# Kernel optimization log

Hardware: AMD Instinct MI355X
Metric: run time of the kernel (lower is better)

Reference implementation:

```python
import math
import jax
import jax.numpy as jnp
import numpy as np

DIM = 1024
NUM_EXPERTS = 4
CAPACITY = (0.25, 0.25, 0.25, 0.25)
BATCH = 8
NUM_TOKENS = 4096


def setup_inputs() -> dict:
    key = jax.random.key(0)
    k1, k2 = jax.random.split(key)
    input_tokens = jax.random.normal(k1, (BATCH, NUM_TOKENS, DIM), dtype=jnp.float32)
    # torch Linear weight [out_features, in_features], init uniform(-0.02, 0.02), bias zeros
    W = jax.random.uniform(k2, (NUM_EXPERTS, DIM), dtype=jnp.float32, minval=-0.02, maxval=0.02)
    b = jnp.zeros((NUM_EXPERTS,), dtype=jnp.float32)
    return {"input_tokens": input_tokens, "W": W, "b": b}


def reference(input_tokens, W, b):
    # router probs in float32 (autocast disabled in original)
    logits = jnp.einsum('bnd,ed->bne', input_tokens, W) + b  # [B, N, E]
    probs = jax.nn.softmax(logits, axis=-1)

    B, N, _ = probs.shape
    token_mask = jnp.full((B, N), -1, dtype=jnp.int32)
    neg_inf = jnp.float32(-jnp.inf)

    # Sequential expert-preferred assignment, highest expert index first.
    for j in reversed(range(NUM_EXPERTS)):
        capacity = int(math.floor(CAPACITY[j] * N))
        if capacity == 0:
            continue
        r_j = jnp.where(token_mask != -1, neg_inf, probs[:, :, j])  # mask already-assigned tokens
        _, topk_idx = jax.lax.top_k(r_j, capacity)  # [B, capacity]
        # Faithful to torch `token_mask[:, topk_indices] = j`: assigns expert j at the
        # union of selected token positions across ALL batch rows (broadcast over dim 0).
        token_mask = token_mask.at[:, topk_idx.reshape(-1)].set(j)

    token_mask = jnp.where(token_mask == -1, 0, token_mask)
    expert_probs = jnp.take_along_axis(probs, token_mask[..., None], axis=2)[..., 0]  # [B, N]
    return token_mask, expert_probs
```

## Files before the change

### kernel.cpp

```cpp
#include <hip/hip_runtime.h>
#include <math.h>

#define DIM 1024
#define NE 4
#define NTOK 4096
#define NB 8
#define CAP 1024
#define NWAVE 16
#define HSTRIDE 257

typedef float fx4 __attribute__((ext_vector_type(4)));

__global__ __launch_bounds__(256) void probs_kernel(const float* __restrict__ tokens,
                                                    const float* __restrict__ W,
                                                    const float* __restrict__ bias,
                                                    float* __restrict__ probs) {
    __shared__ float4 Wl[NE * 256];
    int tid = threadIdx.x;
    const float4* W4 = (const float4*)W;
    for (int i = tid; i < NE * 256; i += 256) Wl[i] = W4[i];
    __syncthreads();

    int wave = tid >> 6, lane = tid & 63;
    long tok = (long)blockIdx.x * 4 + wave;
    const fx4* t4 = (const fx4*)(tokens + tok * DIM);

    double a0 = 0, a1 = 0, a2 = 0, a3 = 0;
#pragma unroll
    for (int kk = 0; kk < 4; kk++) {
        int c = lane + 64 * kk;
        fx4 v = __builtin_nontemporal_load(&t4[c]);
        float4 w0 = Wl[0 * 256 + c];
        float4 w1 = Wl[1 * 256 + c];
        float4 w2 = Wl[2 * 256 + c];
        float4 w3 = Wl[3 * 256 + c];
        a0 += (double)v.x * w0.x + (double)v.y * w0.y + (double)v.z * w0.z + (double)v.w * w0.w;
        a1 += (double)v.x * w1.x + (double)v.y * w1.y + (double)v.z * w1.z + (double)v.w * w1.w;
        a2 += (double)v.x * w2.x + (double)v.y * w2.y + (double)v.z * w2.z + (double)v.w * w2.w;
        a3 += (double)v.x * w3.x + (double)v.y * w3.y + (double)v.z * w3.z + (double)v.w * w3.w;
    }
#pragma unroll
    for (int off = 32; off > 0; off >>= 1) {
        a0 += __shfl_xor(a0, off);
        a1 += __shfl_xor(a1, off);
        a2 += __shfl_xor(a2, off);
        a3 += __shfl_xor(a3, off);
    }
    if (lane == 0) {
        float f0 = (float)(a0 + (double)bias[0]);
        float f1 = (float)(a1 + (double)bias[1]);
        float f2 = (float)(a2 + (double)bias[2]);
        float f3 = (float)(a3 + (double)bias[3]);
        double m = fmax(fmax((double)f0, (double)f1), fmax((double)f2, (double)f3));
        double e0 = exp((double)f0 - m);
        double e1 = exp((double)f1 - m);
        double e2 = exp((double)f2 - m);
        double e3 = exp((double)f3 - m);
        double s = e0 + e1 + e2 + e3;
        float4 p;
        p.x = (float)(e0 / s);
        p.y = (float)(e1 / s);
        p.z = (float)(e2 / s);
        p.w = (float)(e3 / s);
        ((float4*)probs)[tok] = p;
    }
}


__device__ __forceinline__ unsigned block_exscan_1024(unsigned v, unsigned* wl,
                                                      int tid, unsigned* total) {
    int lane = tid & 63, w = tid >> 6;
    unsigned s = v;
#pragma unroll
    for (int off = 1; off < 64; off <<= 1) {
        unsigned t = __shfl_up(s, off);
        if (lane >= off) s += t;
    }
    if (lane == 63) wl[w] = s;
    __syncthreads();
    if (tid < 64) {
        unsigned x = (tid < 16) ? wl[tid] : 0u;
#pragma unroll
        for (int off = 1; off < 16; off <<= 1) {
            unsigned t = __shfl_up(x, off);
            if (lane >= off) x += t;
        }
        if (tid < 16) wl[tid] = x;
    }
    __syncthreads();
    unsigned waveoff = (w == 0) ? 0u : wl[w - 1];
    unsigned tot = wl[15];
    __syncthreads();
    if (total) *total = tot;
    return waveoff + (s - v);
}

__device__ __forceinline__ void radix_select_regs(const unsigned key[4], unsigned cap,
                                                  unsigned* whist, unsigned* hist,
                                                  unsigned* scanb, unsigned* bcast,
                                                  int tid,
                                                  unsigned* v_out, unsigned* rem_out) {
    int w = tid >> 6;
    unsigned* myh = whist + w * HSTRIDE;
    if (tid == 0) { bcast[0] = 0u; bcast[1] = cap; }
#pragma unroll
    for (int shift = 24; shift >= 0; shift -= 8) {
        for (int i = tid; i < NWAVE * HSTRIDE; i += 1024) whist[i] = 0u;
        __syncthreads();
        unsigned pref = bcast[0], rem = bcast[1];
        bool all = (shift == 24);
#pragma unroll
        for (int k = 0; k < 4; k++) {
            if (all || (key[k] >> (shift + 8)) == pref)
                atomicAdd(&myh[(key[k] >> shift) & 255u], 1u);
        }
        __syncthreads();
        if (tid < 256) {
            unsigned s = 0;
#pragma unroll
            for (int w2 = 0; w2 < NWAVE; w2++) s += whist[w2 * HSTRIDE + tid];
            hist[tid] = s;
        }
        __syncthreads();
        if (tid < 64) {
            unsigned h0 = hist[4 * tid], h1 = hist[4 * tid + 1];
            unsigned h2 = hist[4 * tid + 2], h3 = hist[4 * tid + 3];
            unsigned s3 = h3, s2 = h2 + s3, s1 = h1 + s2, s0 = h0 + s1;
            unsigned t = s0, s = t;
#pragma unroll
            for (int off = 1; off < 64; off <<= 1) {
                unsigned o = __shfl_down(s, off);
                if (tid + off < 64) s += o;
            }
            unsigned E = s - t;
            scanb[4 * tid]     = E + s0;
            scanb[4 * tid + 1] = E + s1;
            scanb[4 * tid + 2] = E + s2;
            scanb[4 * tid + 3] = E + s3;
        }
        __syncthreads();
        if (tid < 256) {
            unsigned incl = scanb[tid];
            unsigned excl = (tid < 255) ? scanb[tid + 1] : 0u;
            if (excl < rem && rem <= incl) {
                bcast[0] = (pref << 8) | (unsigned)tid;
                bcast[1] = rem - excl;
            }
        }
        __syncthreads();
    }
    *v_out = bcast[0];
    *rem_out = bcast[1];
}

__device__ __forceinline__ unsigned mono_key(float p) {
    unsigned bits = __float_as_uint(p);
    return (bits & 0x80000000u) ? ~bits : (bits | 0x80000000u);
}

__device__ __forceinline__ void select_to_bitmap(const unsigned key[4], unsigned* bitmap,
                                                 unsigned* whist, unsigned* hist,
                                                 unsigned* scanb, unsigned* bcast,
                                                 unsigned* wl, int tid) {
    unsigned vstar, rem;
    radix_select_regs(key, CAP, whist, hist, scanb, bcast, tid, &vstar, &rem);
    unsigned loc[4], v = 0;
#pragma unroll
    for (int k = 0; k < 4; k++) { loc[k] = (key[k] == vstar); v += loc[k]; }
    unsigned tot;
    unsigned ex = block_exscan_1024(v, wl, tid, &tot);
#pragma unroll
    for (int k = 0; k < 4; k++) {
        int i = 4 * tid + k;
        bool sel = (key[k] > vstar) || (loc[k] && ex < rem);
        ex += loc[k];
        if (sel) atomicOr(&bitmap[i >> 5], 1u << (i & 31));
    }
    __syncthreads();
}

__global__ __launch_bounds__(1024) void select3_kernel(const float* __restrict__ probs,
                                                       unsigned* __restrict__ selbits) {
    __shared__ unsigned whist[NWAVE * HSTRIDE];
    __shared__ unsigned hist[256], scanb[256], bcast[2];
    __shared__ unsigned bitmap[128];
    __shared__ unsigned wl[17];
    int b = blockIdx.x, tid = threadIdx.x;

    const float4* p4 = (const float4*)probs + (size_t)b * NTOK;
    unsigned key[4];
#pragma unroll
    for (int k = 0; k < 4; k++) key[k] = mono_key(p4[4 * tid + k].w);
    if (tid < 128) bitmap[tid] = 0u;

    select_to_bitmap(key, bitmap, whist, hist, scanb, bcast, wl, tid);

    if (tid < 128) selbits[b * 128 + tid] = bitmap[tid];
}

__global__ __launch_bounds__(1024) void rest_kernel(const float* __restrict__ probs,
                                                    const unsigned* __restrict__ selbits,
                                                    int* __restrict__ finalmask) {
    __shared__ int maskv[NTOK];
    __shared__ unsigned whist[NWAVE * HSTRIDE];
    __shared__ unsigned hist[256], scanb[256], bcast[2];
    __shared__ unsigned bitmap[128];
    __shared__ unsigned wl[17];
    int tid = threadIdx.x;

    if (tid < 128) {
        unsigned u = 0;
#pragma unroll
        for (int bb = 0; bb < NB; bb++) u |= selbits[bb * 128 + tid];
        bitmap[tid] = u;
    }
    __syncthreads();
#pragma unroll
    for (int k = 0; k < 4; k++) {
        int i = tid + k * 1024;
        maskv[i] = ((bitmap[i >> 5] >> (i & 31)) & 1u) ? 3 : -1;
    }
    __syncthreads();

    for (int j = 2; j >= 0; j--) {
        unsigned loc[4], v = 0;
#pragma unroll
        for (int k = 0; k < 4; k++) { loc[k] = (maskv[4 * tid + k] != -1); v += loc[k]; }
        unsigned M;
        unsigned ex = block_exscan_1024(v, wl, tid, &M);
        unsigned U = NTOK - M;

        if (U <= CAP) {
            unsigned need = CAP - U;
#pragma unroll
            for (int k = 0; k < 4; k++) {
                int i = 4 * tid + k;
                bool sel = (!loc[k]) || (ex < need);
                ex += loc[k];
                if (sel) maskv[i] = j;
            }
            __syncthreads();
        } else {
            if (tid < 128) bitmap[tid] = 0u;
            __syncthreads();
            for (int bb = 0; bb < NB; bb++) {
                unsigned k2[4];
#pragma unroll
                for (int k = 0; k < 4; k++) {
                    int i = 4 * tid + k;
                    k2[k] = (maskv[i] != -1)
                                ? 0u
                                : mono_key(probs[((size_t)bb * NTOK + i) * NE + j]);
                }
                select_to_bitmap(k2, bitmap, whist, hist, scanb, bcast, wl, tid);
            }
#pragma unroll
            for (int k = 0; k < 4; k++) {
                int i = 4 * tid + k;
                if ((bitmap[i >> 5] >> (i & 31)) & 1u) maskv[i] = j;
            }
            __syncthreads();
        }
    }

#pragma unroll
    for (int k = 0; k < 4; k++) {
        int i = tid + k * 1024;
        int m = maskv[i];
        finalmask[i] = (m < 0) ? 0 : m;
    }
}

__global__ __launch_bounds__(256) void final_kernel(const float* __restrict__ probs,
                                                    const int* __restrict__ fm,
                                                    float* __restrict__ out) {
    int i = blockIdx.x * 256 + threadIdx.x;
    int n = i & (NTOK - 1);
    int m = fm[n];
    out[i] = (float)m;
    out[NB * NTOK + i] = probs[(size_t)i * NE + m];
}

extern "C" void kernel_launch(void* const* d_in, const int* in_sizes, int n_in,
                              void* d_out, int out_size, void* d_ws, size_t ws_size,
                              hipStream_t stream) {
    const float* tokens = (const float*)d_in[0];
    const float* W      = (const float*)d_in[1];
    const float* bias   = (const float*)d_in[2];
    float* out = (float*)d_out;

    float*    probs   = (float*)d_ws;
    unsigned* selbits = (unsigned*)((char*)d_ws + (size_t)NB * NTOK * NE * sizeof(float));
    int*      fmask   = (int*)(selbits + NB * 128);

    probs_kernel<<<(NB * NTOK) / 4, 256, 0, stream>>>(tokens, W, bias, probs);
    select3_kernel<<<NB, 1024, 0, stream>>>(probs, selbits);
    rest_kernel<<<1, 1024, 0, stream>>>(probs, selbits, fmask);
    final_kernel<<<(NB * NTOK) / 256, 256, 0, stream>>>(probs, fmask, out);
}
```

Measured before the change: 211.4 us.

## Keep router weights in registers and process four tokens per wave with prefetch

The router-probability kernel stops staging W in shared memory and loads each lane's weight slice into registers once. Each wave now handles four tokens and prefetches the next token's row while computing the current one, so the grid shrinks by a factor of four. This aims to drop the per-block shared-memory load and barrier and to hide global load latency for the bandwidth-bound token read. In exchange it uses more registers per thread, which may lower occupancy, and leaves fewer blocks in flight.

Result: no change. 211.6 us (+0.1%).

```diff
diff --git a/kernel.cpp b/kernel.cpp
--- a/kernel.cpp
+++ b/kernel.cpp
@@ -15,54 +15,78 @@
                                                     const float* __restrict__ W,
                                                     const float* __restrict__ bias,
                                                     float* __restrict__ probs) {
-    __shared__ float4 Wl[NE * 256];
-    int tid = threadIdx.x;
-    const float4* W4 = (const float4*)W;
-    for (int i = tid; i < NE * 256; i += 256) Wl[i] = W4[i];
-    __syncthreads();
-
+    int tid  = threadIdx.x;
     int wave = tid >> 6, lane = tid & 63;
-    long tok = (long)blockIdx.x * 4 + wave;
-    const fx4* t4 = (const fx4*)(tokens + tok * DIM);
-
-    double a0 = 0, a1 = 0, a2 = 0, a3 = 0;
-#pragma unroll
-    for (int kk = 0; kk < 4; kk++) {
-        int c = lane + 64 * kk;
-        fx4 v = __builtin_nontemporal_load(&t4[c]);
-        float4 w0 = Wl[0 * 256 + c];
-        float4 w1 = Wl[1 * 256 + c];
-        float4 w2 = Wl[2 * 256 + c];
-        float4 w3 = Wl[3 * 256 + c];
-        a0 += (double)v.x * w0.x + (double)v.y * w0.y + (double)v.z * w0.z + (double)v.w * w0.w;
-        a1 += (double)v.x * w1.x + (double)v.y * w1.y + (double)v.z * w1.z + (double)v.w * w1.w;
-        a2 += (double)v.x * w2.x + (double)v.y * w2.y + (double)v.z * w2.z + (double)v.w * w2.w;
-        a3 += (double)v.x * w3.x + (double)v.y * w3.y + (double)v.z * w3.z + (double)v.w * w3.w;
-    }
-#pragma unroll
-    for (int off = 32; off > 0; off >>= 1) {
-        a0 += __shfl_xor(a0, off);
-        a1 += __shfl_xor(a1, off);
-        a2 += __shfl_xor(a2, off);
-        a3 += __shfl_xor(a3, off);
-    }
-    if (lane == 0) {
-        float f0 = (float)(a0 + (double)bias[0]);
-        float f1 = (float)(a1 + (double)bias[1]);
-        float f2 = (float)(a2 + (double)bias[2]);
-        float f3 = (float)(a3 + (double)bias[3]);
-        double m = fmax(fmax((double)f0, (double)f1), fmax((double)f2, (double)f3));
-        double e0 = exp((double)f0 - m);
-        double e1 = exp((double)f1 - m);
-        double e2 = exp((double)f2 - m);
-        double e3 = exp((double)f3 - m);
-        double s = e0 + e1 + e2 + e3;
-        float4 p;
-        p.x = (float)(e0 / s);
-        p.y = (float)(e1 / s);
-        p.z = (float)(e2 / s);
-        p.w = (float)(e3 / s);
-        ((float4*)probs)[tok] = p;
+
+    const fx4* W4 = (const fx4*)W;
+    fx4 w[NE][4];
+#pragma unroll
+    for (int e = 0; e < NE; e++)
+#pragma unroll
+        for (int k = 0; k < 4; k++)
+            w[e][k] = W4[e * 256 + lane + 64 * k];
+
+    double b0 = (double)bias[0], b1 = (double)bias[1];
+    double b2 = (double)bias[2], b3 = (double)bias[3];
+
+    long tok0 = ((long)blockIdx.x * 4 + wave) * 4;
+
+    fx4 v0, v1, v2, v3;
+    {
+        const fx4* tp = (const fx4*)(tokens + tok0 * DIM);
+        v0 = __builtin_nontemporal_load(&tp[lane]);
+        v1 = __builtin_nontemporal_load(&tp[lane + 64]);
+        v2 = __builtin_nontemporal_load(&tp[lane + 128]);
+        v3 = __builtin_nontemporal_load(&tp[lane + 192]);
+    }
+
+#pragma unroll
+    for (int t = 0; t < 4; t++) {
+        fx4 n0, n1, n2, n3;
+        if (t < 3) {
+            const fx4* np = (const fx4*)(tokens + (tok0 + t + 1) * DIM);
+            n0 = __builtin_nontemporal_load(&np[lane]);
+            n1 = __builtin_nontemporal_load(&np[lane + 64]);
+            n2 = __builtin_nontemporal_load(&np[lane + 128]);
+            n3 = __builtin_nontemporal_load(&np[lane + 192]);
+        }
+
+        double a0 = 0, a1 = 0, a2 = 0, a3 = 0;
+        fx4 vv[4] = {v0, v1, v2, v3};
+#pragma unroll
+        for (int k = 0; k < 4; k++) {
+            fx4 v = vv[k];
+            a0 += (double)v.x * w[0][k].x + (double)v.y * w[0][k].y + (double)v.z * w[0][k].z + (double)v.w * w[0][k].w;
+            a1 += (double)v.x * w[1][k].x + (double)v.y * w[1][k].y + (double)v.z * w[1][k].z + (double)v.w * w[1][k].w;
+            a2 += (double)v.x * w[2][k].x + (double)v.y * w[2][k].y + (double)v.z * w[2][k].z + (double)v.w * w[2][k].w;
+            a3 += (double)v.x * w[3][k].x + (double)v.y * w[3][k].y + (double)v.z * w[3][k].z + (double)v.w * w[3][k].w;
+        }
+#pragma unroll
+        for (int off = 32; off > 0; off >>= 1) {
+            a0 += __shfl_xor(a0, off);
+            a1 += __shfl_xor(a1, off);
+            a2 += __shfl_xor(a2, off);
+            a3 += __shfl_xor(a3, off);
+        }
+        if (lane == 0) {
+            float f0 = (float)(a0 + b0);
+            float f1 = (float)(a1 + b1);
+            float f2 = (float)(a2 + b2);
+            float f3 = (float)(a3 + b3);
+            double m = fmax(fmax((double)f0, (double)f1), fmax((double)f2, (double)f3));
+            double e0 = exp((double)f0 - m);
+            double e1 = exp((double)f1 - m);
+            double e2 = exp((double)f2 - m);
+            double e3 = exp((double)f3 - m);
+            double s = e0 + e1 + e2 + e3;
+            float4 p;
+            p.x = (float)(e0 / s);
+            p.y = (float)(e1 / s);
+            p.z = (float)(e2 / s);
+            p.w = (float)(e3 / s);
+            ((float4*)probs)[tok0 + t] = p;
+        }
+        if (t < 3) { v0 = n0; v1 = n1; v2 = n2; v3 = n3; }
     }
 }
 
@@ -293,7 +317,7 @@
     unsigned* selbits = (unsigned*)((char*)d_ws + (size_t)NB * NTOK * NE * sizeof(float));
     int*      fmask   = (int*)(selbits + NB * 128);
 
-    probs_kernel<<<(NB * NTOK) / 4, 256, 0, stream>>>(tokens, W, bias, probs);
+    probs_kernel<<<(NB * NTOK) / 16, 256, 0, stream>>>(tokens, W, bias, probs);
     select3_kernel<<<NB, 1024, 0, stream>>>(probs, selbits);
     rest_kernel<<<1, 1024, 0, stream>>>(probs, selbits, fmask);
     final_kernel<<<(NB * NTOK) / 256, 256, 0, stream>>>(probs, fmask, out);
```
